# Kernel optimization log

Hardware: AMD Instinct MI355X
Metric: run time of the kernel (lower is better)

The kernel has to match this reference:

```python
import jax, jax.numpy as jnp
import numpy as np

B, C, H, W = 4, 256, 64, 64
GROUPS = 32
EPS = 1e-6
N_BITS_QKV = 8
N_BITS_SM = 8


def setup_inputs() -> dict:
    key = jax.random.key(0)
    ks = jax.random.split(key, 6)
    s = 1.0 / np.sqrt(C)
    return {
        "x": jax.random.normal(ks[0], (B, C, H, W), jnp.float32),
        "gn_scale": jnp.ones((C,), jnp.float32),
        "gn_bias": jnp.zeros((C,), jnp.float32),
        "wq": jax.random.normal(ks[1], (C, C), jnp.float32) * s,
        "bq": jnp.zeros((C,), jnp.float32),
        "wk": jax.random.normal(ks[2], (C, C), jnp.float32) * s,
        "bk": jnp.zeros((C,), jnp.float32),
        "wv": jax.random.normal(ks[3], (C, C), jnp.float32) * s,
        "bv": jnp.zeros((C,), jnp.float32),
        "wproj": jax.random.normal(ks[4], (C, C), jnp.float32) * s,
        "bproj": jnp.zeros((C,), jnp.float32),
        # per-tensor uniform-affine quantizer params (delta, zero_point)
        "dq": jnp.float32(8.0 / 255.0), "zq": jnp.float32(128.0),
        "dk": jnp.float32(8.0 / 255.0), "zk": jnp.float32(128.0),
        "dv": jnp.float32(8.0 / 255.0), "zv": jnp.float32(128.0),
        "dw": jnp.float32(1.0 / 255.0), "zw": jnp.float32(0.0),
    }


def ste_round(x):
    # round with straight-through gradient (as in round_ste of BRECQ/QDrop)
    return x + jax.lax.stop_gradient(jnp.round(x) - x)


def fake_quant(x, delta, zero_point, n_bits):
    # UniformAffineQuantizer: quant -> clamp -> dequant
    n_levels = 2 ** n_bits
    x_int = ste_round(x / delta) + zero_point
    x_q = jnp.clip(x_int, 0, n_levels - 1)
    return (x_q - zero_point) * delta


def group_norm(x, scale, bias):
    b, c, h, w = x.shape
    xg = x.reshape(b, GROUPS, (c // GROUPS) * h * w)
    mu = xg.mean(-1, keepdims=True)
    var = xg.var(-1, keepdims=True)
    xn = ((xg - mu) * jax.lax.rsqrt(var + EPS)).reshape(b, c, h, w)
    return xn * scale[None, :, None, None] + bias[None, :, None, None]


def conv1x1(x, w, b):
    # 1x1 conv == channel-mixing matmul
    return jnp.einsum('bchw,oc->bohw', x, w) + b[None, :, None, None]


def reference(x, gn_scale, gn_bias, wq, bq, wk, bk, wv, bv, wproj, bproj,
              dq, zq, dk, zk, dv, zv, dw, zw):
    h_ = group_norm(x, gn_scale, gn_bias)
    q = conv1x1(h_, wq, bq)
    k = conv1x1(h_, wk, bk)
    v = conv1x1(h_, wv, bv)
    b, c, h, w = q.shape
    hw = h * w
    q = q.reshape(b, c, hw).transpose(0, 2, 1)   # [b, hw, c]
    k = k.reshape(b, c, hw)                      # [b, c, hw]
    q = fake_quant(q, dq, zq, N_BITS_QKV)
    k = fake_quant(k, dk, zk, N_BITS_QKV)
    attn = jnp.einsum('bnc,bcm->bnm', q, k) * (c ** -0.5)  # [b, hw, hw]
    attn = jax.nn.softmax(attn, axis=2)
    v = fake_quant(v.reshape(b, c, hw), dv, zv, N_BITS_QKV)
    attn = fake_quant(attn.transpose(0, 2, 1), dw, zw, N_BITS_SM)  # [b, m, n]
    h_out = jnp.einsum('bcm,bmn->bcn', v, attn).reshape(b, c, h, w)
    return x + conv1x1(h_out, wproj, bproj)
```

## Files before the change

### kernel.cpp

```cpp
#include <hip/hip_runtime.h>


#define Bb 4
#define Cc 256
#define Nn 4096
#define NGRP 32
#define LOG2E 1.4426950408889634f

typedef unsigned short u16;
typedef unsigned int   u32;
typedef unsigned char  u8;
typedef __attribute__((ext_vector_type(8))) short bf16x8;
typedef __attribute__((ext_vector_type(4))) float f32x4;
typedef __attribute__((ext_vector_type(4))) int   i32x4;

#define MFMA16(a,b,c)    __builtin_amdgcn_mfma_f32_16x16x32_bf16((a),(b),(c),0,0,0)
#define MFMA_I8(a,b,c)   __builtin_amdgcn_mfma_i32_16x16x64_i8((a),(b),(c),0,0,0)
#define EXP2F(x)         __builtin_amdgcn_exp2f(x)

static __device__ __forceinline__ u16 f2bf(float x){
  u32 u = __float_as_uint(x);
  u += 0x7fffu + ((u >> 16) & 1u);
  return (u16)(u >> 16);
}
static __device__ __forceinline__ float bf2f(u16 h){ return __uint_as_float(((u32)h) << 16); }

union U64c { u16 u[4]; uint2 v; };

__global__ __launch_bounds__(256) void k_gn_stats(const float* __restrict__ x,
                                                  float* __restrict__ mu, float* __restrict__ rs){
  int bg = blockIdx.x;
  const float4* p = (const float4*)(x + (size_t)bg * (8 * Nn));
  float s = 0.f, q = 0.f;
  for (int i = threadIdx.x; i < 8*Nn/4; i += 256){
    float4 v = p[i];
    s += v.x + v.y + v.z + v.w;
    q += v.x*v.x + v.y*v.y + v.z*v.z + v.w*v.w;
  }
  __shared__ float rsum[256], rsq[256];
  rsum[threadIdx.x] = s; rsq[threadIdx.x] = q;
  __syncthreads();
  for (int off = 128; off > 0; off >>= 1){
    if (threadIdx.x < off){ rsum[threadIdx.x] += rsum[threadIdx.x+off]; rsq[threadIdx.x] += rsq[threadIdx.x+off]; }
    __syncthreads();
  }
  if (threadIdx.x == 0){
    const float inv = 1.0f / (8*Nn);
    float m = rsum[0]*inv;
    float var = rsq[0]*inv - m*m;
    mu[bg] = m; rs[bg] = rsqrtf(var + 1e-6f);
  }
}

__global__ __launch_bounds__(256) void k_wsplit(const float* __restrict__ wq, const float* __restrict__ wk,
                                                const float* __restrict__ wv, const float* __restrict__ wp,
                                                u16* __restrict__ WH, u16* __restrict__ WL){
  int gid = blockIdx.x*256 + threadIdx.x;
  int mat = gid >> 16, idx = gid & 65535;
  const float* src = (mat == 0) ? wq : (mat == 1) ? wk : (mat == 2) ? wv : wp;
  float w = src[idx];
  u16 h = f2bf(w);
  WH[gid] = h;
  WL[gid] = f2bf(w - bf2f(h));
}

__global__ __launch_bounds__(1024) void k_convqkv(const float* __restrict__ x,
                                                 const float* __restrict__ gsc, const float* __restrict__ gbi,
                                                 const float* __restrict__ mu, const float* __restrict__ rs,
                                                 const u16* __restrict__ WH, const u16* __restrict__ WL,
                                                 const float* __restrict__ bq, const float* __restrict__ bk,
                                                 const float* __restrict__ bv,
                                                 const float* __restrict__ dq, const float* __restrict__ zq,
                                                 const float* __restrict__ dk, const float* __restrict__ zk,
                                                 const float* __restrict__ dv, const float* __restrict__ zv,
                                                 u8* __restrict__ qT8, u8* __restrict__ kT8,
                                                 u8* __restrict__ v8,
                                                 u32* __restrict__ stat, int* __restrict__ vsum){
  int nt = blockIdx.x, b = blockIdx.y;
  __shared__ u16 Lh[64*256], Ll[64*256];
  __shared__ float yt[64*65];
  __shared__ float sa[256], sb[256];
  __shared__ u32 rowacc[2][64];
  int t = threadIdx.x, lane = t & 63, wave = t >> 6;
  int lo16 = lane & 15, quad = lane >> 4;
  int o0 = wave*16;
  int n0 = nt*64;

  if (t < 256){
    int c = t;
    int bg = b*NGRP + (c >> 3);
    float a = rs[bg] * gsc[c];
    sa[c] = a;
    sb[c] = gbi[c] - mu[bg]*a;
  }
  if (t < 128) rowacc[t >> 6][t & 63] = 0;
  __syncthreads();

  {
    int r  = t >> 4, cq = t & 15;
    int nl = t >> 4, c4 = t & 15;
    #pragma unroll
    for (int ct = 0; ct < 4; ++ct){
      int c0 = ct*64;
      float4 xv = *(const float4*)(x + ((size_t)b*Cc + c0 + r)*Nn + n0 + cq*4);
      float a = sa[c0 + r], bb = sb[c0 + r];
      yt[r*65 + cq*4 + 0] = xv.x*a + bb;
      yt[r*65 + cq*4 + 1] = xv.y*a + bb;
      yt[r*65 + cq*4 + 2] = xv.z*a + bb;
      yt[r*65 + cq*4 + 3] = xv.w*a + bb;
      __syncthreads();
      int cg = c0 + c4*4;
      union { u16 us[4]; uint2 v2; } Ph, Pl;
      #pragma unroll
      for (int uu = 0; uu < 4; ++uu){
        float y = yt[(c4*4 + uu)*65 + nl];
        u16 h = f2bf(y);
        Ph.us[uu] = h; Pl.us[uu] = f2bf(y - bf2f(h));
      }
      int ch = cg >> 3;
      int addr = nl*256 + ((ch ^ (nl & 15)) << 3) + (cg & 7);
      *(uint2*)(Lh + addr) = Ph.v2;
      *(uint2*)(Ll + addr) = Pl.v2;
      __syncthreads();
    }
  }

  f32x4 zf = {0.f,0.f,0.f,0.f};
  f32x4 aQ[4] = {zf, zf, zf, zf};
  f32x4 aK[4] = {zf, zf, zf, zf};
  f32x4 aV[4] = {zf, zf, zf, zf};
  {
    const u16* wbh = WH + (size_t)(o0 + lo16) * 256 + quad*8;
    const u16* wbl = WL + (size_t)(o0 + lo16) * 256 + quad*8;
    #pragma unroll
    for (int k = 0; k < 8; ++k){
      bf16x8 whq = *(const bf16x8*)(wbh + k*32);
      bf16x8 wlq = *(const bf16x8*)(wbl + k*32);
      bf16x8 whk = *(const bf16x8*)(wbh + 65536 + k*32);
      bf16x8 wlk = *(const bf16x8*)(wbl + 65536 + k*32);
      bf16x8 whv = *(const bf16x8*)(wbh + 131072 + k*32);
      bf16x8 wlv = *(const bf16x8*)(wbl + 131072 + k*32);
      #pragma unroll
      for (int ns = 0; ns < 4; ++ns){
        int r = ns*16 + lo16;
        int ph = ((k*4 + quad) ^ (r & 15)) * 8;
        bf16x8 bh = *(const bf16x8*)(Lh + r*256 + ph);
        bf16x8 bl = *(const bf16x8*)(Ll + r*256 + ph);
        aQ[ns] = MFMA16(whq, bh, aQ[ns]);
        aK[ns] = MFMA16(whk, bh, aK[ns]);
        aV[ns] = MFMA16(whv, bh, aV[ns]);
        aQ[ns] = MFMA16(wlq, bh, aQ[ns]);
        aK[ns] = MFMA16(wlk, bh, aK[ns]);
        aV[ns] = MFMA16(wlv, bh, aV[ns]);
        aQ[ns] = MFMA16(whq, bl, aQ[ns]);
        aK[ns] = MFMA16(whk, bl, aK[ns]);
        aV[ns] = MFMA16(whv, bl, aV[ns]);
      }
    }
  }

  {
    float bia[4];
    #pragma unroll
    for (int r = 0; r < 4; ++r) bia[r] = bq[o0 + quad*4 + r];
    float z = zq[0]; float invd = 1.0f / dq[0];
    #pragma unroll
    for (int ns = 0; ns < 4; ++ns){
      int n = nt*64 + ns*16 + lo16;
      u32 wpk = 0;
      int nrm = 0;
      #pragma unroll
      for (int r = 0; r < 4; ++r){
        float v = aQ[ns][r] + bia[r];
        float xq = fminf(fmaxf(rintf(v*invd) + z, 0.f), 255.f);
        int qi = (int)rintf(xq - z);
        nrm += qi*qi;
        wpk |= ((u32)(qi & 255)) << (8*r);
      }
      *(u32*)(qT8 + ((size_t)b*Nn + n)*Cc + o0 + quad*4) = wpk;
      nrm += __shfl_xor(nrm, 16, 64);
      nrm += __shfl_xor(nrm, 32, 64);
      if (lane < 16) atomicAdd(&rowacc[0][ns*16 + lo16], (u32)nrm);
    }
  }
  {
    float bia[4];
    #pragma unroll
    for (int r = 0; r < 4; ++r) bia[r] = bk[o0 + quad*4 + r];
    float z = zk[0]; float invd = 1.0f / dk[0];
    #pragma unroll
    for (int ns = 0; ns < 4; ++ns){
      int n = nt*64 + ns*16 + lo16;
      u32 wpk = 0;
      int nrm = 0;
      #pragma unroll
      for (int r = 0; r < 4; ++r){
        float v = aK[ns][r] + bia[r];
        float xq = fminf(fmaxf(rintf(v*invd) + z, 0.f), 255.f);
        int qi = (int)rintf(xq - z);
        nrm += qi*qi;
        wpk |= ((u32)(qi & 255)) << (8*r);
      }
      *(u32*)(kT8 + ((size_t)b*Nn + n)*Cc + o0 + quad*4) = wpk;
      nrm += __shfl_xor(nrm, 16, 64);
      nrm += __shfl_xor(nrm, 32, 64);
      if (lane < 16) atomicAdd(&rowacc[1][ns*16 + lo16], (u32)nrm);
    }
  }
  {
    float bia[4];
    #pragma unroll
    for (int r = 0; r < 4; ++r) bia[r] = bv[o0 + quad*4 + r];
    float z = zv[0]; float invd = 1.0f / dv[0];
    int vpart[4] = {0, 0, 0, 0};
    #pragma unroll
    for (int ns = 0; ns < 4; ++ns){
      int n = nt*64 + ns*16 + lo16;
      #pragma unroll
      for (int r = 0; r < 4; ++r){
        float v = aV[ns][r] + bia[r];
        float xq = fminf(fmaxf(rintf(v*invd) + z, 0.f), 255.f);
        int qi = (int)rintf(xq - z);
        vpart[r] += qi;
        v8[((size_t)b*Cc + o0 + quad*4 + r)*Nn + n] = (u8)(qi & 255);
      }
    }
    #pragma unroll
    for (int r = 0; r < 4; ++r){
      #pragma unroll
      for (int m = 1; m < 16; m <<= 1)
        vpart[r] += __shfl_xor(vpart[r], m, 64);
    }
    if (lo16 == 0){
      #pragma unroll
      for (int r = 0; r < 4; ++r)
        atomicAdd(&vsum[b*Cc + o0 + quad*4 + r], vpart[r]);
    }
  }

  __syncthreads();
  if (wave < 2){
    u32 v = rowacc[wave][lane];
    #pragma unroll
    for (int m = 1; m < 64; m <<= 1){
      u32 o = (u32)__shfl_xor((int)v, m, 64);
      v = v > o ? v : o;
    }
    if (lane == 0) atomicMax(&stat[wave*4 + b], v);
  }
}

__global__ __launch_bounds__(1024) void k_qpv(const u8* __restrict__ qT8, const u8* __restrict__ kT8,
                                              const u8* __restrict__ v8,
                                              const u32* __restrict__ stat,
                                              const float* __restrict__ pdq, const float* __restrict__ pdk,
                                              const float* __restrict__ pdw, const float* __restrict__ pzw,
                                              const int* __restrict__ vsum,
                                              const float* __restrict__ pdv,
                                              const u16* __restrict__ WH, const u16* __restrict__ WL,
                                              const float* __restrict__ bp,
                                              const float* __restrict__ xres,
                                              float* __restrict__ outF){
  int nt = blockIdx.x, b = blockIdx.y;
  __shared__ alignas(16) u8  Kt[2][2][64*256];
  __shared__ alignas(16) u32 Pt[2][2][64*16];
  __shared__ float Lbuf[4][4][16];
  int t = threadIdx.x, lane = t & 63, w = t >> 6;
  int lo16 = lane & 15, q = lane >> 4;
  int ms = w & 3, nsq = w >> 2;

  float sc2 = pdq[0]*pdk[0]*0.0625f*LOG2E;
  float M2 = sc2 * sqrtf((float)stat[b] * (float)stat[4+b]);
  float zw = pzw[0];

  i32x4 qf[4];
  {
    const u8* qb = qT8 + ((size_t)b*Nn + nt*64 + nsq*16 + lo16)*256;
    #pragma unroll
    for (int kk = 0; kk < 4; ++kk)
      qf[kk] = *(const i32x4*)(qb + kk*64 + q*16);
  }

  int krow = t >> 4, kch = t & 15;
  int kdst = krow*256 + ((kch ^ (krow & 15)) << 4);
  const u8* kb = kT8 + (size_t)b*Nn*256;

  int mrow = ms*16 + lo16;
  int kofs[4];
  #pragma unroll
  for (int kk = 0; kk < 4; ++kk) kofs[kk] = mrow*256 + (((kk*4 + q) ^ (mrow & 15)) << 4);

  const u8* vp = v8 + ((size_t)(b*Cc + w*16 + lo16))*Nn + q*16;

  float lr = 0.f;
  {
    const u8* kld = kb + (size_t)krow*256 + kch*16;
    uint4 kr0 = *(const uint4*)(kld);
    uint4 kr1 = *(const uint4*)(kld + 16384);
    *(uint4*)(Kt[0][0] + kdst) = kr0;
    *(uint4*)(Kt[0][1] + kdst) = kr1;
    kld += 2*16384;
    kr0 = *(const uint4*)(kld);
    kr1 = *(const uint4*)(kld + 16384);
    kld += 2*16384;
    __syncthreads();
    i32x4 spA0, spB0, spA1, spB1;
    #pragma unroll 2
    for (int i = 0; i < 32; ++i){
      int cur = i & 1;
      i32x4 sA0 = {0,0,0,0}, sB0 = {0,0,0,0}, sA1 = {0,0,0,0}, sB1 = {0,0,0,0};
      sA0 = MFMA_I8(*(const i32x4*)(Kt[cur][0] + kofs[0]), qf[0], sA0);
      sB0 = MFMA_I8(*(const i32x4*)(Kt[cur][0] + kofs[1]), qf[1], sB0);
      sA1 = MFMA_I8(*(const i32x4*)(Kt[cur][1] + kofs[0]), qf[0], sA1);
      sB1 = MFMA_I8(*(const i32x4*)(Kt[cur][1] + kofs[1]), qf[1], sB1);
      sA0 = MFMA_I8(*(const i32x4*)(Kt[cur][0] + kofs[2]), qf[2], sA0);
      sB0 = MFMA_I8(*(const i32x4*)(Kt[cur][0] + kofs[3]), qf[3], sB0);
      sA1 = MFMA_I8(*(const i32x4*)(Kt[cur][1] + kofs[2]), qf[2], sA1);
      sB1 = MFMA_I8(*(const i32x4*)(Kt[cur][1] + kofs[3]), qf[3], sB1);
      if (i < 31){
        *(uint4*)(Kt[cur ^ 1][0] + kdst) = kr0;
        *(uint4*)(Kt[cur ^ 1][1] + kdst) = kr1;
        if (i < 30){
          kr0 = *(const uint4*)(kld);
          kr1 = *(const uint4*)(kld + 16384);
          kld += 2*16384;
        }
      }
      if (i > 0){
        #pragma unroll
        for (int r = 0; r < 4; ++r){
          lr += EXP2F(fmaf((float)(spA0[r] + spB0[r]), sc2, -M2));
          lr += EXP2F(fmaf((float)(spA1[r] + spB1[r]), sc2, -M2));
        }
      }
      spA0 = sA0; spB0 = sB0; spA1 = sA1; spB1 = sB1;
      __syncthreads();
    }
    #pragma unroll
    for (int r = 0; r < 4; ++r){
      lr += EXP2F(fmaf((float)(spA0[r] + spB0[r]), sc2, -M2));
      lr += EXP2F(fmaf((float)(spA1[r] + spB1[r]), sc2, -M2));
    }
  }
  lr += __shfl_xor(lr, 16, 64);
  lr += __shfl_xor(lr, 32, 64);
  if (lane < 16) Lbuf[nsq][ms][lo16] = lr;
  __syncthreads();
  float Ls = Lbuf[nsq][0][lo16] + Lbuf[nsq][1][lo16] + Lbuf[nsq][2][lo16] + Lbuf[nsq][3][lo16];
  float crn = __log2f(1.0f / (pdw[0] * Ls)) - M2;

  i32x4 zi = {0,0,0,0};
  i32x4 acc[4] = {zi,zi,zi,zi};
  int nrow = nsq*16 + lo16;
  int pdst = nrow*16 + ((ms ^ (nrow & 3) ^ ((nrow >> 2) & 3)) << 2) + q;
  int pofs[4];
  #pragma unroll
  for (int ns = 0; ns < 4; ++ns){
    int pr = ns*16 + lo16;
    pofs[ns] = pr*16 + ((q ^ (pr & 3) ^ ((pr >> 2) & 3)) << 2);
  }
  {
    const u8* kld = kb + (size_t)krow*256 + kch*16;
    uint4 kr0 = *(const uint4*)(kld);
    uint4 kr1 = *(const uint4*)(kld + 16384);
    *(uint4*)(Kt[0][0] + kdst) = kr0;
    *(uint4*)(Kt[0][1] + kdst) = kr1;
    kld += 2*16384;
    kr0 = *(const uint4*)(kld);
    kr1 = *(const uint4*)(kld + 16384);
    kld += 2*16384;
    const u8* vld = vp + 128;
    i32x4 af0 = *(const i32x4*)(vp);
    i32x4 af1 = *(const i32x4*)(vp + 64);
    i32x4 af0p, af1p, af0pp, af1pp;
    i32x4 spA0, spB0, spA1, spB1;
    __syncthreads();
    #pragma unroll 2
    for (int i = 0; i < 32; ++i){
      int cur = i & 1;
      i32x4 sA0 = {0,0,0,0}, sB0 = {0,0,0,0}, sA1 = {0,0,0,0}, sB1 = {0,0,0,0};
      sA0 = MFMA_I8(*(const i32x4*)(Kt[cur][0] + kofs[0]), qf[0], sA0);
      sB0 = MFMA_I8(*(const i32x4*)(Kt[cur][0] + kofs[1]), qf[1], sB0);
      sA1 = MFMA_I8(*(const i32x4*)(Kt[cur][1] + kofs[0]), qf[0], sA1);
      sB1 = MFMA_I8(*(const i32x4*)(Kt[cur][1] + kofs[1]), qf[1], sB1);
      sA0 = MFMA_I8(*(const i32x4*)(Kt[cur][0] + kofs[2]), qf[2], sA0);
      sB0 = MFMA_I8(*(const i32x4*)(Kt[cur][0] + kofs[3]), qf[3], sB0);
      sA1 = MFMA_I8(*(const i32x4*)(Kt[cur][1] + kofs[2]), qf[2], sA1);
      sB1 = MFMA_I8(*(const i32x4*)(Kt[cur][1] + kofs[3]), qf[3], sB1);
      if (i < 31){
        *(uint4*)(Kt[cur ^ 1][0] + kdst) = kr0;
        *(uint4*)(Kt[cur ^ 1][1] + kdst) = kr1;
        if (i < 30){
          kr0 = *(const uint4*)(kld);
          kr1 = *(const uint4*)(kld + 16384);
          kld += 2*16384;
        }
      }
      if (i > 1){
        acc[0] = MFMA_I8(af0pp, *(const i32x4*)(Pt[cur][0] + pofs[0]), acc[0]);
        acc[1] = MFMA_I8(af0pp, *(const i32x4*)(Pt[cur][0] + pofs[1]), acc[1]);
        acc[2] = MFMA_I8(af0pp, *(const i32x4*)(Pt[cur][0] + pofs[2]), acc[2]);
        acc[3] = MFMA_I8(af0pp, *(const i32x4*)(Pt[cur][0] + pofs[3]), acc[3]);
        acc[0] = MFMA_I8(af1pp, *(const i32x4*)(Pt[cur][1] + pofs[0]), acc[0]);
        acc[1] = MFMA_I8(af1pp, *(const i32x4*)(Pt[cur][1] + pofs[1]), acc[1]);
        acc[2] = MFMA_I8(af1pp, *(const i32x4*)(Pt[cur][1] + pofs[2]), acc[2]);
        acc[3] = MFMA_I8(af1pp, *(const i32x4*)(Pt[cur][1] + pofs[3]), acc[3]);
      }
      if (i > 0){
        u32 wp0 = 0, wp1 = 0;
        #pragma unroll
        for (int r = 0; r < 4; ++r){
          float at0 = EXP2F(fmaf((float)(spA0[r] + spB0[r]), sc2, crn));
          float y0 = fminf(fmaxf(rintf(at0) + zw, 0.f), 255.f);
          wp0 = __builtin_amdgcn_cvt_pk_u8_f32(y0, (u32)r, wp0);
          float at1 = EXP2F(fmaf((float)(spA1[r] + spB1[r]), sc2, crn));
          float y1 = fminf(fmaxf(rintf(at1) + zw, 0.f), 255.f);
          wp1 = __builtin_amdgcn_cvt_pk_u8_f32(y1, (u32)r, wp1);
        }
        Pt[cur ^ 1][0][pdst] = wp0 ^ 0x80808080u;
        Pt[cur ^ 1][1][pdst] = wp1 ^ 0x80808080u;
      }
      spA0 = sA0; spB0 = sB0; spA1 = sA1; spB1 = sB1;
      af0pp = af0p; af0p = af0; af1pp = af1p; af1p = af1;
      if (i < 31){
        af0 = *(const i32x4*)(vld);
        af1 = *(const i32x4*)(vld + 64);
        vld += 128;
      }
      __syncthreads();
    }
    acc[0] = MFMA_I8(af0pp, *(const i32x4*)(Pt[0][0] + pofs[0]), acc[0]);
    acc[1] = MFMA_I8(af0pp, *(const i32x4*)(Pt[0][0] + pofs[1]), acc[1]);
    acc[2] = MFMA_I8(af0pp, *(const i32x4*)(Pt[0][0] + pofs[2]), acc[2]);
    acc[3] = MFMA_I8(af0pp, *(const i32x4*)(Pt[0][0] + pofs[3]), acc[3]);
    acc[0] = MFMA_I8(af1pp, *(const i32x4*)(Pt[0][1] + pofs[0]), acc[0]);
    acc[1] = MFMA_I8(af1pp, *(const i32x4*)(Pt[0][1] + pofs[1]), acc[1]);
    acc[2] = MFMA_I8(af1pp, *(const i32x4*)(Pt[0][1] + pofs[2]), acc[2]);
    acc[3] = MFMA_I8(af1pp, *(const i32x4*)(Pt[0][1] + pofs[3]), acc[3]);
    {
      u32 wp0 = 0, wp1 = 0;
      #pragma unroll
      for (int r = 0; r < 4; ++r){
        float at0 = EXP2F(fmaf((float)(spA0[r] + spB0[r]), sc2, crn));
        float y0 = fminf(fmaxf(rintf(at0) + zw, 0.f), 255.f);
        wp0 = __builtin_amdgcn_cvt_pk_u8_f32(y0, (u32)r, wp0);
        float at1 = EXP2F(fmaf((float)(spA1[r] + spB1[r]), sc2, crn));
        float y1 = fminf(fmaxf(rintf(at1) + zw, 0.f), 255.f);
        wp1 = __builtin_amdgcn_cvt_pk_u8_f32(y1, (u32)r, wp1);
      }
      Pt[1][0][pdst] = wp0 ^ 0x80808080u;
      Pt[1][1][pdst] = wp1 ^ 0x80808080u;
    }
    __syncthreads();
    acc[0] = MFMA_I8(af0p, *(const i32x4*)(Pt[1][0] + pofs[0]), acc[0]);
    acc[1] = MFMA_I8(af0p, *(const i32x4*)(Pt[1][0] + pofs[1]), acc[1]);
    acc[2] = MFMA_I8(af0p, *(const i32x4*)(Pt[1][0] + pofs[2]), acc[2]);
    acc[3] = MFMA_I8(af0p, *(const i32x4*)(Pt[1][0] + pofs[3]), acc[3]);
    acc[0] = MFMA_I8(af1p, *(const i32x4*)(Pt[1][1] + pofs[0]), acc[0]);
    acc[1] = MFMA_I8(af1p, *(const i32x4*)(Pt[1][1] + pofs[1]), acc[1]);
    acc[2] = MFMA_I8(af1p, *(const i32x4*)(Pt[1][1] + pofs[2]), acc[2]);
    acc[3] = MFMA_I8(af1p, *(const i32x4*)(Pt[1][1] + pofs[3]), acc[3]);
  }

  u16* Ht = (u16*)Kt;
  {
    float s = pdv[0] * pdw[0];
    float corr = s * (128.0f - zw);
    int c0 = w*16 + q*4;
    int kc0 = c0 >> 7;
    int ch8 = (c0 >> 3) & 15;
    int c4  = c0 & 7;
    float cv[4];
    #pragma unroll
    for (int r = 0; r < 4; ++r) cv[r] = corr * (float)vsum[b*Cc + c0 + r];
    #pragma unroll
    for (int ns = 0; ns < 4; ++ns){
      int rrow = ns*16 + lo16;
      U64c Uh;
      #pragma unroll
      for (int r = 0; r < 4; ++r)
        Uh.u[r] = f2bf(s*(float)acc[ns][r] + cv[r]);
      *(uint2*)(Ht + rrow*256 + kc0*128 + ((ch8 ^ (rrow & 7)) << 3) + c4) = Uh.v;
    }
  }
  __syncthreads();
  {
    f32x4 zf = {0.f,0.f,0.f,0.f};
    f32x4 acc2[4] = {zf, zf, zf, zf};
    const u16* wbh = WH + (size_t)3*65536 + (size_t)(w*16 + lo16)*256 + q*8;
    const u16* wbl = WL + (size_t)3*65536 + (size_t)(w*16 + lo16)*256 + q*8;
    #pragma unroll
    for (int kc = 0; kc < 2; ++kc){
      bf16x8 ah[4], al[4];
      #pragma unroll
      for (int k4 = 0; k4 < 4; ++k4){
        ah[k4] = *(const bf16x8*)(wbh + kc*128 + k4*32);
        al[k4] = *(const bf16x8*)(wbl + kc*128 + k4*32);
      }
      #pragma unroll
      for (int k4 = 0; k4 < 4; ++k4){
        #pragma unroll
        for (int ns = 0; ns < 4; ++ns){
          int rrow = ns*16 + lo16;
          bf16x8 bh = *(const bf16x8*)(Ht + rrow*256 + kc*128 + (((k4*4 + q) ^ (rrow & 7)) << 3));
          acc2[ns] = MFMA16(ah[k4], bh, acc2[ns]);
          acc2[ns] = MFMA16(al[k4], bh, acc2[ns]);
        }
      }
    }
    float bia[4];
    #pragma unroll
    for (int r = 0; r < 4; ++r) bia[r] = bp[w*16 + q*4 + r];
    #pragma unroll
    for (int ns = 0; ns < 4; ++ns){
      int n = nt*64 + ns*16 + lo16;
      #pragma unroll
      for (int r = 0; r < 4; ++r){
        size_t a = ((size_t)b*Cc + w*16 + q*4 + r)*Nn + n;
        outF[a] = xres[a] + acc2[ns][r] + bia[r];
      }
    }
  }
}

extern "C" void kernel_launch(void* const* d_in, const int* in_sizes, int n_in,
                              void* d_out, int out_size, void* d_ws, size_t ws_size,
                              hipStream_t stream){
  (void)in_sizes; (void)n_in; (void)out_size; (void)ws_size;
  const float* x   = (const float*)d_in[0];
  const float* gsc = (const float*)d_in[1];
  const float* gbi = (const float*)d_in[2];
  const float* wq  = (const float*)d_in[3];
  const float* bq  = (const float*)d_in[4];
  const float* wk  = (const float*)d_in[5];
  const float* bk  = (const float*)d_in[6];
  const float* wv  = (const float*)d_in[7];
  const float* bv  = (const float*)d_in[8];
  const float* wp  = (const float*)d_in[9];
  const float* bp  = (const float*)d_in[10];
  const float* dq  = (const float*)d_in[11];
  const float* zq  = (const float*)d_in[12];
  const float* dk  = (const float*)d_in[13];
  const float* zk  = (const float*)d_in[14];
  const float* dv  = (const float*)d_in[15];
  const float* zv  = (const float*)d_in[16];
  const float* dw  = (const float*)d_in[17];
  const float* zw  = (const float*)d_in[18];
  float* out = (float*)d_out;

  const size_t SZT = (size_t)Bb*Nn*Cc;
  u16* hT_hi = (u16*)d_ws;
  u16* hT_lo = hT_hi + SZT;
  u16* h2    = hT_lo + SZT;
  u8*  qT8   = (u8*)(h2 + SZT);
  u8*  kT8   = qT8 + SZT;
  u8*  v8    = kT8 + SZT;
  u16* WH    = (u16*)(v8 + SZT);
  u16* WL    = WH + 4*65536;
  float* mu  = (float*)(WL + 4*65536);
  float* rs  = mu + 128;
  u32*  stat = (u32*)(rs + 128);
  int*  vsum = (int*)(stat + 8);

  k_gn_stats<<<dim3(Bb*NGRP), 256, 0, stream>>>(x, mu, rs);
  k_wsplit<<<dim3(1024), 256, 0, stream>>>(wq, wk, wv, wp, WH, WL);
  hipMemsetAsync(stat, 0, (8 + Bb*Cc)*sizeof(u32), stream);

  k_convqkv<<<dim3(Nn/64, Bb), 1024, 0, stream>>>(x, gsc, gbi, mu, rs, WH, WL,
                                                  bq, bk, bv, dq, zq, dk, zk, dv, zv,
                                                  qT8, kT8, v8, stat, vsum);

  k_qpv<<<dim3(Nn/64, Bb), 1024, 0, stream>>>(qT8, kT8, v8, stat, dq, dk, dw, zw, vsum, dv,
                                              WH, WL, bp, x, out);
}
```

Measured before the change: 240.8 us.

## Load K tiles via direct global-to-LDS loads with pre-swizzled layout; merge prep kernels

K tiles in the attention kernel are now fetched with global_load_lds straight into shared memory, skipping the register staging and the separate LDS stores. To keep the bank-conflict-avoiding XOR swizzle, the conv kernel now writes kT8 in a pre-swizzled channel order, so a linear copy lands in the swizzled LDS layout. The GN-stats, weight-split and stat-memset steps are merged into one prep launch to cut launch overhead. The risk is correctness if the swizzle mapping does not match the LDS read offsets, and the async LDS loads now depend only on the existing barriers for ordering.

```diff
diff --git a/kernel.cpp b/kernel.cpp
--- a/kernel.cpp
+++ b/kernel.cpp
@@ -25,43 +25,53 @@
 }
 static __device__ __forceinline__ float bf2f(u16 h){ return __uint_as_float(((u32)h) << 16); }
 
+static __device__ __forceinline__ void gload_lds16(const u8* g, u8* l){
+  __builtin_amdgcn_global_load_lds((const __attribute__((address_space(1))) void*)g,
+                                   (__attribute__((address_space(3))) void*)l, 16, 0, 0);
+}
+
 union U64c { u16 u[4]; uint2 v; };
 
-__global__ __launch_bounds__(256) void k_gn_stats(const float* __restrict__ x,
-                                                  float* __restrict__ mu, float* __restrict__ rs){
-  int bg = blockIdx.x;
-  const float4* p = (const float4*)(x + (size_t)bg * (8 * Nn));
-  float s = 0.f, q = 0.f;
-  for (int i = threadIdx.x; i < 8*Nn/4; i += 256){
-    float4 v = p[i];
-    s += v.x + v.y + v.z + v.w;
-    q += v.x*v.x + v.y*v.y + v.z*v.z + v.w*v.w;
-  }
-  __shared__ float rsum[256], rsq[256];
-  rsum[threadIdx.x] = s; rsq[threadIdx.x] = q;
-  __syncthreads();
-  for (int off = 128; off > 0; off >>= 1){
-    if (threadIdx.x < off){ rsum[threadIdx.x] += rsum[threadIdx.x+off]; rsq[threadIdx.x] += rsq[threadIdx.x+off]; }
+__global__ __launch_bounds__(256) void k_prep(const float* __restrict__ x,
+                                              float* __restrict__ mu, float* __restrict__ rs,
+                                              const float* __restrict__ wq, const float* __restrict__ wk,
+                                              const float* __restrict__ wv, const float* __restrict__ wp,
+                                              u16* __restrict__ WH, u16* __restrict__ WL,
+                                              u32* __restrict__ statz){
+  int bid = blockIdx.x;
+  if (bid < 128){
+    int bg = bid;
+    const float4* p = (const float4*)(x + (size_t)bg * (8 * Nn));
+    float s = 0.f, q = 0.f;
+    for (int i = threadIdx.x; i < 8*Nn/4; i += 256){
+      float4 v = p[i];
+      s += v.x + v.y + v.z + v.w;
+      q += v.x*v.x + v.y*v.y + v.z*v.z + v.w*v.w;
+    }
+    __shared__ float rsum[256], rsq[256];
+    rsum[threadIdx.x] = s; rsq[threadIdx.x] = q;
     __syncthreads();
-  }
-  if (threadIdx.x == 0){
-    const float inv = 1.0f / (8*Nn);
-    float m = rsum[0]*inv;
-    float var = rsq[0]*inv - m*m;
-    mu[bg] = m; rs[bg] = rsqrtf(var + 1e-6f);
-  }
-}
-
-__global__ __launch_bounds__(256) void k_wsplit(const float* __restrict__ wq, const float* __restrict__ wk,
-                                                const float* __restrict__ wv, const float* __restrict__ wp,
-                                                u16* __restrict__ WH, u16* __restrict__ WL){
-  int gid = blockIdx.x*256 + threadIdx.x;
-  int mat = gid >> 16, idx = gid & 65535;
-  const float* src = (mat == 0) ? wq : (mat == 1) ? wk : (mat == 2) ? wv : wp;
-  float w = src[idx];
-  u16 h = f2bf(w);
-  WH[gid] = h;
-  WL[gid] = f2bf(w - bf2f(h));
+    for (int off = 128; off > 0; off >>= 1){
+      if (threadIdx.x < off){ rsum[threadIdx.x] += rsum[threadIdx.x+off]; rsq[threadIdx.x] += rsq[threadIdx.x+off]; }
+      __syncthreads();
+    }
+    if (threadIdx.x == 0){
+      const float inv = 1.0f / (8*Nn);
+      float m = rsum[0]*inv;
+      float var = rsq[0]*inv - m*m;
+      mu[bg] = m; rs[bg] = rsqrtf(var + 1e-6f);
+    }
+  } else if (bid < 1152){
+    int gid = (bid - 128)*256 + threadIdx.x;
+    int mat = gid >> 16, idx = gid & 65535;
+    const float* src = (mat == 0) ? wq : (mat == 1) ? wk : (mat == 2) ? wv : wp;
+    float w = src[idx];
+    u16 h = f2bf(w);
+    WH[gid] = h;
+    WL[gid] = f2bf(w - bf2f(h));
+  } else {
+    for (int j = threadIdx.x; j < 8 + Bb*Cc; j += 256) statz[j] = 0;
+  }
 }
 
 __global__ __launch_bounds__(1024) void k_convqkv(const float* __restrict__ x,
@@ -188,6 +198,7 @@
     #pragma unroll
     for (int r = 0; r < 4; ++r) bia[r] = bk[o0 + quad*4 + r];
     float z = zk[0]; float invd = 1.0f / dk[0];
+    int swofs = ((wave ^ lo16) << 4) + quad*4;
     #pragma unroll
     for (int ns = 0; ns < 4; ++ns){
       int n = nt*64 + ns*16 + lo16;
@@ -201,7 +212,7 @@
         nrm += qi*qi;
         wpk |= ((u32)(qi & 255)) << (8*r);
       }
-      *(u32*)(kT8 + ((size_t)b*Nn + n)*Cc + o0 + quad*4) = wpk;
+      *(u32*)(kT8 + ((size_t)b*Nn + n)*Cc + swofs) = wpk;
       nrm += __shfl_xor(nrm, 16, 64);
       nrm += __shfl_xor(nrm, 32, 64);
       if (lane < 16) atomicAdd(&rowacc[1][ns*16 + lo16], (u32)nrm);
@@ -281,9 +292,8 @@
       qf[kk] = *(const i32x4*)(qb + kk*64 + q*16);
   }
 
-  int krow = t >> 4, kch = t & 15;
-  int kdst = krow*256 + ((kch ^ (krow & 15)) << 4);
   const u8* kb = kT8 + (size_t)b*Nn*256;
+  int wofs = w*1024;
 
   int mrow = ms*16 + lo16;
   int kofs[4];
@@ -294,20 +304,20 @@
 
   float lr = 0.f;
   {
-    const u8* kld = kb + (size_t)krow*256 + kch*16;
-    uint4 kr0 = *(const uint4*)(kld);
-    uint4 kr1 = *(const uint4*)(kld + 16384);
-    *(uint4*)(Kt[0][0] + kdst) = kr0;
-    *(uint4*)(Kt[0][1] + kdst) = kr1;
-    kld += 2*16384;
-    kr0 = *(const uint4*)(kld);
-    kr1 = *(const uint4*)(kld + 16384);
-    kld += 2*16384;
+    const u8* kg = kb + t*16;
+    gload_lds16(kg,         Kt[0][0] + wofs);
+    gload_lds16(kg + 16384, Kt[0][1] + wofs);
+    kg += 32768;
     __syncthreads();
     i32x4 spA0, spB0, spA1, spB1;
     #pragma unroll 2
     for (int i = 0; i < 32; ++i){
       int cur = i & 1;
+      if (i < 31){
+        gload_lds16(kg,         Kt[cur ^ 1][0] + wofs);
+        gload_lds16(kg + 16384, Kt[cur ^ 1][1] + wofs);
+        kg += 32768;
+      }
       i32x4 sA0 = {0,0,0,0}, sB0 = {0,0,0,0}, sA1 = {0,0,0,0}, sB1 = {0,0,0,0};
       sA0 = MFMA_I8(*(const i32x4*)(Kt[cur][0] + kofs[0]), qf[0], sA0);
       sB0 = MFMA_I8(*(const i32x4*)(Kt[cur][0] + kofs[1]), qf[1], sB0);
@@ -317,15 +327,6 @@
       sB0 = MFMA_I8(*(const i32x4*)(Kt[cur][0] + kofs[3]), qf[3], sB0);
       sA1 = MFMA_I8(*(const i32x4*)(Kt[cur][1] + kofs[2]), qf[2], sA1);
       sB1 = MFMA_I8(*(const i32x4*)(Kt[cur][1] + kofs[3]), qf[3], sB1);
-      if (i < 31){
-        *(uint4*)(Kt[cur ^ 1][0] + kdst) = kr0;
-        *(uint4*)(Kt[cur ^ 1][1] + kdst) = kr1;
-        if (i < 30){
-          kr0 = *(const uint4*)(kld);
-          kr1 = *(const uint4*)(kld + 16384);
-          kld += 2*16384;
-        }
-      }
       if (i > 0){
         #pragma unroll
         for (int r = 0; r < 4; ++r){
@@ -360,15 +361,10 @@
     pofs[ns] = pr*16 + ((q ^ (pr & 3) ^ ((pr >> 2) & 3)) << 2);
   }
   {
-    const u8* kld = kb + (size_t)krow*256 + kch*16;
-    uint4 kr0 = *(const uint4*)(kld);
-    uint4 kr1 = *(const uint4*)(kld + 16384);
-    *(uint4*)(Kt[0][0] + kdst) = kr0;
-    *(uint4*)(Kt[0][1] + kdst) = kr1;
-    kld += 2*16384;
-    kr0 = *(const uint4*)(kld);
-    kr1 = *(const uint4*)(kld + 16384);
-    kld += 2*16384;
+    const u8* kg = kb + t*16;
+    gload_lds16(kg,         Kt[0][0] + wofs);
+    gload_lds16(kg + 16384, Kt[0][1] + wofs);
+    kg += 32768;
     const u8* vld = vp + 128;
     i32x4 af0 = *(const i32x4*)(vp);
     i32x4 af1 = *(const i32x4*)(vp + 64);
@@ -378,6 +374,11 @@
     #pragma unroll 2
     for (int i = 0; i < 32; ++i){
       int cur = i & 1;
+      if (i < 31){
+        gload_lds16(kg,         Kt[cur ^ 1][0] + wofs);
+        gload_lds16(kg + 16384, Kt[cur ^ 1][1] + wofs);
+        kg += 32768;
+      }
       i32x4 sA0 = {0,0,0,0}, sB0 = {0,0,0,0}, sA1 = {0,0,0,0}, sB1 = {0,0,0,0};
       sA0 = MFMA_I8(*(const i32x4*)(Kt[cur][0] + kofs[0]), qf[0], sA0);
       sB0 = MFMA_I8(*(const i32x4*)(Kt[cur][0] + kofs[1]), qf[1], sB0);
@@ -387,15 +388,6 @@
       sB0 = MFMA_I8(*(const i32x4*)(Kt[cur][0] + kofs[3]), qf[3], sB0);
       sA1 = MFMA_I8(*(const i32x4*)(Kt[cur][1] + kofs[2]), qf[2], sA1);
       sB1 = MFMA_I8(*(const i32x4*)(Kt[cur][1] + kofs[3]), qf[3], sB1);
-      if (i < 31){
-        *(uint4*)(Kt[cur ^ 1][0] + kdst) = kr0;
-        *(uint4*)(Kt[cur ^ 1][1] + kdst) = kr1;
-        if (i < 30){
-          kr0 = *(const uint4*)(kld);
-          kr1 = *(const uint4*)(kld + 16384);
-          kld += 2*16384;
-        }
-      }
       if (i > 1){
         acc[0] = MFMA_I8(af0pp, *(const i32x4*)(Pt[cur][0] + pofs[0]), acc[0]);
         acc[1] = MFMA_I8(af0pp, *(const i32x4*)(Pt[cur][0] + pofs[1]), acc[1]);
@@ -562,9 +554,7 @@
   u32*  stat = (u32*)(rs + 128);
   int*  vsum = (int*)(stat + 8);
 
-  k_gn_stats<<<dim3(Bb*NGRP), 256, 0, stream>>>(x, mu, rs);
-  k_wsplit<<<dim3(1024), 256, 0, stream>>>(wq, wk, wv, wp, WH, WL);
-  hipMemsetAsync(stat, 0, (8 + Bb*Cc)*sizeof(u32), stream);
+  k_prep<<<dim3(1153), 256, 0, stream>>>(x, mu, rs, wq, wk, wv, wp, WH, WL, stat);
 
   k_convqkv<<<dim3(Nn/64, Bb), 1024, 0, stream>>>(x, gsc, gbi, mu, rs, WH, WL,
                                                   bq, bk, bv, dq, zq, dk, zk, dv, zv,
```

Result: slower. 249.3 us (+3.5%).
